# Optimization experiments

Measured on AMD Instinct MI355X. Metric: run time of the kernel, lower is better.

## Reference

```python
import jax, jax.numpy as jnp
import numpy as np

USER_NUM = 100000
ITEM_NUM = 50000
EMBED = 128
NUM_LAYERS = 3
N_INTERACTIONS = 1000000
BATCH = 16384


def setup_inputs() -> dict:
    key = jax.random.key(0)
    k1, k2 = jax.random.split(key)
    uEmbd = jax.random.normal(k1, (USER_NUM, EMBED), dtype=jnp.float32) * 0.01
    iEmbd = jax.random.normal(k2, (ITEM_NUM, EMBED), dtype=jnp.float32) * 0.01

    # Build symmetric normalized Laplacian L = D^-1/2 A D^-1/2 in COO form,
    # mirroring buildLaplacianMat (A holds ratings; D from binary degree).
    rng = np.random.default_rng(0)
    users = rng.integers(0, USER_NUM, N_INTERACTIONS)
    items = rng.integers(0, ITEM_NUM, N_INTERACTIONS)
    ratings = rng.integers(1, 6, N_INTERACTIONS).astype(np.float32)
    N = USER_NUM + ITEM_NUM
    row = np.concatenate([users, USER_NUM + items]).astype(np.int32)
    col = np.concatenate([USER_NUM + items, users]).astype(np.int32)
    vals = np.concatenate([ratings, ratings])
    deg = np.bincount(row, minlength=N).astype(np.float32)
    deg = np.maximum(deg, 1.0)
    vals = vals / np.sqrt(deg[row] * deg[col])

    k3, k4 = jax.random.split(jax.random.fold_in(key, 1))
    userIdx = jax.random.randint(k3, (BATCH,), 0, USER_NUM, dtype=jnp.int32)
    itemIdx = jax.random.randint(k4, (BATCH,), 0, ITEM_NUM, dtype=jnp.int32)

    return {
        "uEmbd": uEmbd,
        "iEmbd": iEmbd,
        "L_val": jnp.asarray(vals, dtype=jnp.float32),
        "L_row": jnp.asarray(row),
        "L_col": jnp.asarray(col),
        "userIdx": userIdx,
        "itemIdx": itemIdx,
    }


def reference(uEmbd, iEmbd, L_val, L_row, L_col, userIdx, itemIdx):
    userNum = uEmbd.shape[0]
    N = userNum + iEmbd.shape[0]
    # [N, d] stacked user+item embeddings
    feats = jnp.concatenate([uEmbd, iEmbd], axis=0)
    acc = feats  # running sum over layer outputs (layer 0 included)
    h = feats
    for _ in range(NUM_LAYERS):
        # SpMM: h <- L @ h via gather + segment-sum over COO edges
        h = jax.ops.segment_sum(L_val[:, None] * h[L_col], L_row, num_segments=N)
        acc = acc + h
    final = acc / jnp.asarray(NUM_LAYERS + 1, dtype=feats.dtype)
    u = final[userIdx]                       # [B, d]
    v = final[itemIdx + userNum]             # [B, d]
    return jnp.sum(u * v, axis=1)            # [B]
```

## Files before the change

### kernel.cpp

```cpp
#include <hip/hip_runtime.h>
#include <hip/hip_fp16.h>

#define EMBED 128
#define CHUNK 8
#define T_TILE 4096
#define NB_SH 10
#define BCAP 32768



__global__ __launch_bounds__(256) void passA(const int* __restrict__ row,
                                             const int* __restrict__ col,
                                             const float* __restrict__ val,
                                             int* __restrict__ bcnt,
                                             long long* __restrict__ bedges, int E) {
    __shared__ int sh_scan[256];
    __shared__ int sh_start[256];
    __shared__ int sh_cur[256];
    __shared__ int sh_base[256];
    __shared__ long long sh_data[T_TILE];
    __shared__ int sh_gpos[T_TILE];
    const int t0  = blockIdx.x * T_TILE;
    const int tid = threadIdx.x;

    sh_scan[tid] = 0;
    __syncthreads();
    #pragma unroll
    for (int i = 0; i < T_TILE / 256; ++i) {
        int idx = t0 + i * 256 + tid;
        if (idx < E) atomicAdd(&sh_scan[row[idx] >> NB_SH], 1);
    }
    __syncthreads();
    int x = sh_scan[tid];
    __syncthreads();
    for (int off = 1; off < 256; off <<= 1) {
        int t = (tid >= off) ? sh_scan[tid - off] : 0;
        __syncthreads();
        sh_scan[tid] += t;
        __syncthreads();
    }
    int excl = sh_scan[tid] - x;
    sh_start[tid] = excl;
    sh_cur[tid]   = excl;
    sh_base[tid]  = (x > 0) ? (tid * BCAP + atomicAdd(&bcnt[tid], x)) : 0;
    __syncthreads();
    #pragma unroll
    for (int i = 0; i < T_TILE / 256; ++i) {
        int idx = t0 + i * 256 + tid;
        if (idx < E) {
            int   r = row[idx];
            int   c = col[idx];
            float v = val[idx];
            int   b = r >> NB_SH;
            int   p = atomicAdd(&sh_cur[b], 1);
            unsigned lo = (unsigned)(((r & ((1 << NB_SH) - 1)) << 18) | c);
            sh_data[p] = ((long long)__float_as_int(v) << 32) | (long long)lo;
            sh_gpos[p] = sh_base[b] + (p - sh_start[b]);
        }
    }
    __syncthreads();
    int tot = sh_scan[255];
    for (int p = tid; p < tot; p += 256) {
        bedges[sh_gpos[p]] = sh_data[p];
    }
}


__global__ __launch_bounds__(1024) void passB(const long long* __restrict__ bedges,
                                              const int* __restrict__ bcnt,
                                              int* __restrict__ rs,
                                              int2* __restrict__ edges,
                                              int N, int E, int nbuckets) {
    __shared__ int sh_hist[1024];
    __shared__ int sh_scan[1024];
    __shared__ int sh_bc[256];
    __shared__ int sh_gbase;
    const int b    = blockIdx.x;
    const int tid  = threadIdx.x;
    const int base = b << NB_SH;
    const int cnt  = bcnt[b];
    const long long* seg = bedges + (size_t)b * BCAP;

    sh_hist[tid] = 0;
    if (tid < nbuckets) sh_bc[tid] = bcnt[tid];
    __syncthreads();
    if (tid == 0) {
        int g = 0;
        for (int j = 0; j < b; ++j) g += sh_bc[j];
        sh_gbase = g;
    }
    for (int k = tid; k < cnt; k += 1024) {
        unsigned lo = (unsigned)seg[k];
        atomicAdd(&sh_hist[lo >> 18], 1);
    }
    __syncthreads();
    int x = sh_hist[tid];
    sh_scan[tid] = x;
    __syncthreads();
    for (int off = 1; off < 1024; off <<= 1) {
        int t = (tid >= off) ? sh_scan[tid - off] : 0;
        __syncthreads();
        sh_scan[tid] += t;
        __syncthreads();
    }
    int excl = sh_scan[tid] - x;
    int gbase = sh_gbase;
    int rrow = base + tid;
    if (rrow < N) rs[rrow] = gbase + excl;
    if (b == nbuckets - 1 && tid == 0) rs[N] = E;
    sh_hist[tid] = excl;
    __syncthreads();
    for (int k = tid; k < cnt; k += 1024) {
        long long be = seg[k];
        unsigned lo = (unsigned)be;
        int p = atomicAdd(&sh_hist[lo >> 18], 1);
        edges[gbase + p] = make_int2((int)(lo & 0x3FFFF), (int)(be >> 32));
    }
}


__global__ void f32_to_i8_all(const float* __restrict__ uE, const float* __restrict__ iE,
                              unsigned* __restrict__ dst, float* __restrict__ sc,
                              int userNum, int N) {
    int gid  = blockIdx.x * blockDim.x + threadIdx.x;
    int wave = gid >> 6;
    int lane = threadIdx.x & 63;
    int half = lane >> 5;
    int l32  = lane & 31;
    int row  = wave * 2 + half;
    if (row >= N) return;
    const float* src = (row < userNum) ? (uE + (size_t)row * EMBED)
                                       : (iE + (size_t)(row - userNum) * EMBED);
    float4 a = *(const float4*)(src + 4 * l32);
    float am = fmaxf(fmaxf(fabsf(a.x), fabsf(a.y)), fmaxf(fabsf(a.z), fabsf(a.w)));
    #pragma unroll
    for (int off = 16; off > 0; off >>= 1)
        am = fmaxf(am, __shfl_xor(am, off));
    float s   = am * (1.f / 127.f);
    float inv = (am > 0.f) ? (127.f / am) : 0.f;
    int q0 = (int)rintf(a.x * inv) + 128;
    int q1 = (int)rintf(a.y * inv) + 128;
    int q2 = (int)rintf(a.z * inv) + 128;
    int q3 = (int)rintf(a.w * inv) + 128;
    unsigned w = (unsigned)q0 | ((unsigned)q1 << 8) | ((unsigned)q2 << 16)
               | ((unsigned)q3 << 24);
    dst[(size_t)row * 32 + l32] = w;
    if (l32 == 0) sc[row] = s;
}


#define GATHER_LOOP_I8(HSRC, SCSRC)                                           \
    for (int t = s; t < e; t += 32) {                                         \
        int ecl = t + l32;                                                    \
        ecl = (ecl < e) ? ecl : (e - 1);                                      \
        int2 myed = edges[ecl];                                               \
        float mvs = __int_as_float(myed.y) * SCSRC[myed.x];                   \
        int nb = e - t;                                                       \
        nb = (nb < 32) ? nb : 32;                                             \
        for (int k = 0; k < nb; k += CHUNK) {                                 \
            unsigned raw[CHUNK];                                              \
            float tv[CHUNK];                                                  \
            _Pragma("unroll")                                                 \
            for (int j = 0; j < CHUNK; ++j) {                                 \
                int   c  = __shfl(myed.x, k + j, 32);                         \
                float tj = __shfl(mvs, k + j, 32);                            \
                bool ok  = (k + j) < nb;                                      \
                tv[j]    = ok ? tj : 0.f;                                     \
                raw[j]   = HSRC[(size_t)c * 32 + l32];                        \
            }                                                                 \
            _Pragma("unroll")                                                 \
            for (int j = 0; j < CHUNK; ++j) {                                 \
                unsigned r = raw[j];                                          \
                float tj = tv[j];                                             \
                cb += tj;                                                     \
                acc.x = fmaf((float)(unsigned char)(r),       tj, acc.x);     \
                acc.y = fmaf((float)(unsigned char)(r >> 8),  tj, acc.y);     \
                acc.z = fmaf((float)(unsigned char)(r >> 16), tj, acc.z);     \
                acc.w = fmaf((float)(unsigned char)(r >> 24), tj, acc.w);     \
            }                                                                 \
        }                                                                     \
    }


__global__ void spmm_kernel(const int* __restrict__ rs, const int2* __restrict__ edges,
                            const unsigned* __restrict__ hin,
                            const float* __restrict__ scin,
                            unsigned* __restrict__ hout, float* __restrict__ scout,
                            int N) {
    int gid  = blockIdx.x * blockDim.x + threadIdx.x;
    int wave = gid >> 6;
    int lane = threadIdx.x & 63;
    int half = lane >> 5;
    int l32  = lane & 31;
    int row  = wave * 2 + half;
    if (row >= N) return;
    int s = rs[row], e = rs[row + 1];
    float4 acc = make_float4(0.f, 0.f, 0.f, 0.f);
    float cb = 0.f;

    GATHER_LOOP_I8(hin, scin)

    float b = 128.f * cb;
    acc.x -= b; acc.y -= b; acc.z -= b; acc.w -= b;
    float am = fmaxf(fmaxf(fabsf(acc.x), fabsf(acc.y)), fmaxf(fabsf(acc.z), fabsf(acc.w)));
    #pragma unroll
    for (int off = 16; off > 0; off >>= 1)
        am = fmaxf(am, __shfl_xor(am, off));
    float sq  = am * (1.f / 127.f);
    float inv = (am > 0.f) ? (127.f / am) : 0.f;
    int q0 = (int)rintf(acc.x * inv) + 128;
    int q1 = (int)rintf(acc.y * inv) + 128;
    int q2 = (int)rintf(acc.z * inv) + 128;
    int q3 = (int)rintf(acc.w * inv) + 128;
    unsigned w = (unsigned)q0 | ((unsigned)q1 << 8) | ((unsigned)q2 << 16)
               | ((unsigned)q3 << 24);
    hout[(size_t)row * 32 + l32] = w;
    if (l32 == 0) scout[row] = sq;
}


__global__ void spmm_pair(const int* __restrict__ rs, const int2* __restrict__ edges,
                          const unsigned* __restrict__ h1, const float* __restrict__ sc1,
                          const unsigned* __restrict__ h2, const float* __restrict__ sc2,
                          const float* __restrict__ uE, const float* __restrict__ iE,
                          const int* __restrict__ uIdx, const int* __restrict__ vIdx,
                          float* __restrict__ out, int B, int userNum) {
    int gid  = blockIdx.x * blockDim.x + threadIdx.x;
    int wave = gid >> 6;
    int lane = threadIdx.x & 63;
    int half = lane >> 5;
    int l32  = lane & 31;
    if (wave >= B) return;
    int row;
    const float* emb;
    if (half == 0) {
        int u = uIdx[wave];
        row = u;
        emb = uE + (size_t)u * EMBED;
    } else {
        int it = vIdx[wave];
        row = userNum + it;
        emb = iE + (size_t)it * EMBED;
    }
    float4 acc = *(const float4*)(emb + 4 * l32);
    {
        unsigned r1 = h1[(size_t)row * 32 + l32];
        unsigned r2 = h2[(size_t)row * 32 + l32];
        float s1 = sc1[row];
        float s2 = sc2[row];
        acc.x += ((float)(unsigned char)(r1)       - 128.f) * s1
               + ((float)(unsigned char)(r2)       - 128.f) * s2;
        acc.y += ((float)(unsigned char)(r1 >> 8)  - 128.f) * s1
               + ((float)(unsigned char)(r2 >> 8)  - 128.f) * s2;
        acc.z += ((float)(unsigned char)(r1 >> 16) - 128.f) * s1
               + ((float)(unsigned char)(r2 >> 16) - 128.f) * s2;
        acc.w += ((float)(unsigned char)(r1 >> 24) - 128.f) * s1
               + ((float)(unsigned char)(r2 >> 24) - 128.f) * s2;
    }
    float cb = 0.f;
    int s = rs[row], e = rs[row + 1];

    GATHER_LOOP_I8(h2, sc2)

    float b = 128.f * cb;
    acc.x -= b; acc.y -= b; acc.z -= b; acc.w -= b;

    float ox = __shfl_xor(acc.x, 32);
    float oy = __shfl_xor(acc.y, 32);
    float oz = __shfl_xor(acc.z, 32);
    float ow = __shfl_xor(acc.w, 32);
    float sdot = acc.x * ox + acc.y * oy + acc.z * oz + acc.w * ow;
    #pragma unroll
    for (int off = 16; off > 0; off >>= 1) sdot += __shfl_down(sdot, off, 32);
    sdot += __shfl_down(sdot, 32);
    if (lane == 0) out[wave] = sdot * (1.f / 32.f);
}


extern "C" void kernel_launch(void* const* d_in, const int* in_sizes, int n_in,
                              void* d_out, int out_size, void* d_ws, size_t ws_size,
                              hipStream_t stream) {
    const float* uE      = (const float*)d_in[0];
    const float* iE      = (const float*)d_in[1];
    const float* L_val   = (const float*)d_in[2];
    const int*   L_row   = (const int*)d_in[3];
    const int*   L_col   = (const int*)d_in[4];
    const int*   userIdx = (const int*)d_in[5];
    const int*   itemIdx = (const int*)d_in[6];

    const int userNum = in_sizes[0] / EMBED;
    const int itemNum = in_sizes[1] / EMBED;
    const int N = userNum + itemNum;
    const int E = in_sizes[2];
    const int B = in_sizes[5];
    float* out = (float*)d_out;

    char* ws = (char*)d_ws;
    size_t off = 0;
    auto alloc = [&](size_t bytes) -> void* {
        void* p = ws + off;
        off += (bytes + 1023) & ~(size_t)1023;
        return p;
    };
    const int NBUCKETS = (N + (1 << NB_SH) - 1) >> NB_SH;
    unsigned* h0 = (unsigned*)alloc((size_t)N * EMBED);
    unsigned* h1 = (unsigned*)alloc((size_t)N * EMBED);
    unsigned* h2 = (unsigned*)alloc((size_t)N * EMBED);
    float* sc0   = (float*)alloc((size_t)N * 4);
    float* sc1   = (float*)alloc((size_t)N * 4);
    float* sc2   = (float*)alloc((size_t)N * 4);
    int2*   edges  = (int2*) alloc((size_t)E * 8 + 256);
    long long* bedges = (long long*)alloc((size_t)NBUCKETS * BCAP * 8);
    int*    rs     = (int*)  alloc((size_t)(N + 1) * 4);
    int*    bcnt   = (int*)  alloc(1024);
    (void)off; (void)ws_size; (void)n_in; (void)out_size;

    const int tb = 256;

    (void)hipMemsetAsync(bcnt, 0, 1024, stream);
    passA<<<(E + T_TILE - 1) / T_TILE, 256, 0, stream>>>(L_row, L_col, L_val,
                                                         bcnt, bedges, E);
    passB<<<NBUCKETS, 1024, 0, stream>>>(bedges, bcnt, rs, edges, N, E, NBUCKETS);

    const int cv_blocks = (N + 7) / 8;
    f32_to_i8_all<<<cv_blocks, 256, 0, stream>>>(uE, iE, h0, sc0, userNum, N);

    const int spmm_blocks = (N + 7) / 8;
    spmm_kernel<<<spmm_blocks, 256, 0, stream>>>(rs, edges, h0, sc0, h1, sc1, N);
    spmm_kernel<<<spmm_blocks, 256, 0, stream>>>(rs, edges, h1, sc1, h2, sc2, N);

    spmm_pair<<<(B + 3) / 4, 256, 0, stream>>>(rs, edges, h1, sc1, h2, sc2, uE, iE,
                                               userIdx, itemIdx, out, B, userNum);
}
```

Baseline: 303.4 us.

## Merge SpMM layers into persistent kernel with grid barriers and fuse conversion into passA

The int8 conversion of the embeddings now runs as extra blocks inside the edge-bucketing kernel, which removes one launch. The two SpMM layers and the final pair-dot step are merged into one persistent kernel of 1024 blocks that loops over row-blocks and uses a software grid barrier (atomic counter plus spin) between phases. This replaces three launches and their gaps with in-kernel barriers. In exchange it relies on all 1024 blocks being co-resident and has fewer waves in flight per phase than the full launches had. The barrier counter is zeroed by widening the existing memset, which assumes the counter sits right after bcnt in the workspace.

```diff
diff --git a/kernel.cpp b/kernel.cpp
--- a/kernel.cpp
+++ b/kernel.cpp
@@ -6,22 +6,58 @@
 #define T_TILE 4096
 #define NB_SH 10
 #define BCAP 32768
-
-
-
-__global__ __launch_bounds__(256) void passA(const int* __restrict__ row,
-                                             const int* __restrict__ col,
-                                             const float* __restrict__ val,
-                                             int* __restrict__ bcnt,
-                                             long long* __restrict__ bedges, int E) {
+#define GRIDBLKS 1024
+
+
+
+__global__ __launch_bounds__(256) void passA_cvt(const int* __restrict__ row,
+                                                 const int* __restrict__ col,
+                                                 const float* __restrict__ val,
+                                                 int* __restrict__ bcnt,
+                                                 long long* __restrict__ bedges, int E,
+                                                 const float* __restrict__ uE,
+                                                 const float* __restrict__ iE,
+                                                 unsigned* __restrict__ h0,
+                                                 float* __restrict__ sc0,
+                                                 int userNum, int N, int CA) {
     __shared__ int sh_scan[256];
     __shared__ int sh_start[256];
     __shared__ int sh_cur[256];
     __shared__ int sh_base[256];
     __shared__ long long sh_data[T_TILE];
     __shared__ int sh_gpos[T_TILE];
-    const int t0  = blockIdx.x * T_TILE;
     const int tid = threadIdx.x;
+
+    if ((int)blockIdx.x >= CA) {
+        int vb   = (int)blockIdx.x - CA;
+        int gid  = vb * 256 + tid;
+        int wave = gid >> 6;
+        int lane = tid & 63;
+        int half = lane >> 5;
+        int l32  = lane & 31;
+        int r    = wave * 2 + half;
+        if (r >= N) return;
+        const float* src = (r < userNum) ? (uE + (size_t)r * EMBED)
+                                         : (iE + (size_t)(r - userNum) * EMBED);
+        float4 a = *(const float4*)(src + 4 * l32);
+        float am = fmaxf(fmaxf(fabsf(a.x), fabsf(a.y)), fmaxf(fabsf(a.z), fabsf(a.w)));
+        #pragma unroll
+        for (int off = 16; off > 0; off >>= 1)
+            am = fmaxf(am, __shfl_xor(am, off));
+        float s   = am * (1.f / 127.f);
+        float inv = (am > 0.f) ? (127.f / am) : 0.f;
+        int q0 = (int)rintf(a.x * inv) + 128;
+        int q1 = (int)rintf(a.y * inv) + 128;
+        int q2 = (int)rintf(a.z * inv) + 128;
+        int q3 = (int)rintf(a.w * inv) + 128;
+        unsigned w = (unsigned)q0 | ((unsigned)q1 << 8) | ((unsigned)q2 << 16)
+                   | ((unsigned)q3 << 24);
+        h0[(size_t)r * 32 + l32] = w;
+        if (l32 == 0) sc0[r] = s;
+        return;
+    }
+
+    const int t0 = blockIdx.x * T_TILE;
 
     sh_scan[tid] = 0;
     __syncthreads();
@@ -116,36 +152,6 @@
         int p = atomicAdd(&sh_hist[lo >> 18], 1);
         edges[gbase + p] = make_int2((int)(lo & 0x3FFFF), (int)(be >> 32));
     }
-}
-
-
-__global__ void f32_to_i8_all(const float* __restrict__ uE, const float* __restrict__ iE,
-                              unsigned* __restrict__ dst, float* __restrict__ sc,
-                              int userNum, int N) {
-    int gid  = blockIdx.x * blockDim.x + threadIdx.x;
-    int wave = gid >> 6;
-    int lane = threadIdx.x & 63;
-    int half = lane >> 5;
-    int l32  = lane & 31;
-    int row  = wave * 2 + half;
-    if (row >= N) return;
-    const float* src = (row < userNum) ? (uE + (size_t)row * EMBED)
-                                       : (iE + (size_t)(row - userNum) * EMBED);
-    float4 a = *(const float4*)(src + 4 * l32);
-    float am = fmaxf(fmaxf(fabsf(a.x), fabsf(a.y)), fmaxf(fabsf(a.z), fabsf(a.w)));
-    #pragma unroll
-    for (int off = 16; off > 0; off >>= 1)
-        am = fmaxf(am, __shfl_xor(am, off));
-    float s   = am * (1.f / 127.f);
-    float inv = (am > 0.f) ? (127.f / am) : 0.f;
-    int q0 = (int)rintf(a.x * inv) + 128;
-    int q1 = (int)rintf(a.y * inv) + 128;
-    int q2 = (int)rintf(a.z * inv) + 128;
-    int q3 = (int)rintf(a.w * inv) + 128;
-    unsigned w = (unsigned)q0 | ((unsigned)q1 << 8) | ((unsigned)q2 << 16)
-               | ((unsigned)q3 << 24);
-    dst[(size_t)row * 32 + l32] = w;
-    if (l32 == 0) sc[row] = s;
 }
 
 
@@ -182,14 +188,14 @@
     }
 
 
-__global__ void spmm_kernel(const int* __restrict__ rs, const int2* __restrict__ edges,
-                            const unsigned* __restrict__ hin,
-                            const float* __restrict__ scin,
-                            unsigned* __restrict__ hout, float* __restrict__ scout,
-                            int N) {
-    int gid  = blockIdx.x * blockDim.x + threadIdx.x;
+__device__ __forceinline__ void spmm_rows(int gid, const int* __restrict__ rs,
+                                          const int2* __restrict__ edges,
+                                          const unsigned* __restrict__ hin,
+                                          const float* __restrict__ scin,
+                                          unsigned* __restrict__ hout,
+                                          float* __restrict__ scout, int N) {
     int wave = gid >> 6;
-    int lane = threadIdx.x & 63;
+    int lane = gid & 63;
     int half = lane >> 5;
     int l32  = lane & 31;
     int row  = wave * 2 + half;
@@ -218,16 +224,19 @@
     if (l32 == 0) scout[row] = sq;
 }
 
-
-__global__ void spmm_pair(const int* __restrict__ rs, const int2* __restrict__ edges,
-                          const unsigned* __restrict__ h1, const float* __restrict__ sc1,
-                          const unsigned* __restrict__ h2, const float* __restrict__ sc2,
-                          const float* __restrict__ uE, const float* __restrict__ iE,
-                          const int* __restrict__ uIdx, const int* __restrict__ vIdx,
-                          float* __restrict__ out, int B, int userNum) {
-    int gid  = blockIdx.x * blockDim.x + threadIdx.x;
+__device__ __forceinline__ void pair_rows(int gid, const int* __restrict__ rs,
+                                          const int2* __restrict__ edges,
+                                          const unsigned* __restrict__ h1,
+                                          const float* __restrict__ sc1,
+                                          const unsigned* __restrict__ h2,
+                                          const float* __restrict__ sc2,
+                                          const float* __restrict__ uE,
+                                          const float* __restrict__ iE,
+                                          const int* __restrict__ uIdx,
+                                          const int* __restrict__ vIdx,
+                                          float* __restrict__ out, int B, int userNum) {
     int wave = gid >> 6;
-    int lane = threadIdx.x & 63;
+    int lane = gid & 63;
     int half = lane >> 5;
     int l32  = lane & 31;
     if (wave >= B) return;
@@ -274,6 +283,44 @@
     for (int off = 16; off > 0; off >>= 1) sdot += __shfl_down(sdot, off, 32);
     sdot += __shfl_down(sdot, 32);
     if (lane == 0) out[wave] = sdot * (1.f / 32.f);
+}
+
+
+__device__ __forceinline__ void gridbar(int* bar, int target) {
+    __syncthreads();
+    if (threadIdx.x == 0) {
+        __threadfence();
+        atomicAdd(bar, 1);
+        while (__hip_atomic_load(bar, __ATOMIC_ACQUIRE,
+                                 __HIP_MEMORY_SCOPE_AGENT) < target)
+            __builtin_amdgcn_s_sleep(2);
+        __threadfence();
+    }
+    __syncthreads();
+}
+
+
+__global__ __launch_bounds__(256, 4) void spmm_mega(
+        const int* __restrict__ rs, const int2* __restrict__ edges,
+        const unsigned* __restrict__ h0, const float* __restrict__ sc0,
+        unsigned* __restrict__ h1, float* __restrict__ sc1,
+        unsigned* __restrict__ h2, float* __restrict__ sc2,
+        const float* __restrict__ uE, const float* __restrict__ iE,
+        const int* __restrict__ uIdx, const int* __restrict__ vIdx,
+        float* __restrict__ out, int B, int userNum, int N,
+        int* __restrict__ bar) {
+    const int tid = threadIdx.x;
+    const int nvb = (N + 7) / 8;
+    for (int vb = blockIdx.x; vb < nvb; vb += gridDim.x)
+        spmm_rows(vb * 256 + tid, rs, edges, h0, sc0, h1, sc1, N);
+    gridbar(bar, gridDim.x);
+    for (int vb = blockIdx.x; vb < nvb; vb += gridDim.x)
+        spmm_rows(vb * 256 + tid, rs, edges, h1, sc1, h2, sc2, N);
+    gridbar(bar, 2 * gridDim.x);
+    const int npb = (B + 3) / 4;
+    for (int vb = blockIdx.x; vb < npb; vb += gridDim.x)
+        pair_rows(vb * 256 + tid, rs, edges, h1, sc1, h2, sc2, uE, iE,
+                  uIdx, vIdx, out, B, userNum);
 }
 
 
@@ -313,22 +360,18 @@
     long long* bedges = (long long*)alloc((size_t)NBUCKETS * BCAP * 8);
     int*    rs     = (int*)  alloc((size_t)(N + 1) * 4);
     int*    bcnt   = (int*)  alloc(1024);
+    int*    bar    = (int*)  alloc(1024);
     (void)off; (void)ws_size; (void)n_in; (void)out_size;
 
-    const int tb = 256;
-
-    (void)hipMemsetAsync(bcnt, 0, 1024, stream);
-    passA<<<(E + T_TILE - 1) / T_TILE, 256, 0, stream>>>(L_row, L_col, L_val,
-                                                         bcnt, bedges, E);
+    (void)hipMemsetAsync(bcnt, 0, 2048, stream);
+
+    const int CA  = (E + T_TILE - 1) / T_TILE;
+    const int CVB = (N + 7) / 8;
+    passA_cvt<<<CA + CVB, 256, 0, stream>>>(L_row, L_col, L_val, bcnt, bedges, E,
+                                            uE, iE, h0, sc0, userNum, N, CA);
     passB<<<NBUCKETS, 1024, 0, stream>>>(bedges, bcnt, rs, edges, N, E, NBUCKETS);
 
-    const int cv_blocks = (N + 7) / 8;
-    f32_to_i8_all<<<cv_blocks, 256, 0, stream>>>(uE, iE, h0, sc0, userNum, N);
-
-    const int spmm_blocks = (N + 7) / 8;
-    spmm_kernel<<<spmm_blocks, 256, 0, stream>>>(rs, edges, h0, sc0, h1, sc1, N);
-    spmm_kernel<<<spmm_blocks, 256, 0, stream>>>(rs, edges, h1, sc1, h2, sc2, N);
-
-    spmm_pair<<<(B + 3) / 4, 256, 0, stream>>>(rs, edges, h1, sc1, h2, sc2, uE, iE,
-                                               userIdx, itemIdx, out, B, userNum);
-}
+    spmm_mega<<<GRIDBLKS, 256, 0, stream>>>(rs, edges, h0, sc0, h1, sc1, h2, sc2,
+                                            uE, iE, userIdx, itemIdx, out,
+                                            B, userNum, N, bar);
+}
```

Result: slower. 848.8 us (+179.7%).

## Replace bucketed two-pass CSR build with degree count, scan, and atomic scatter

Applied to the files above, without the earlier changes.

Swaps the shared-memory bucketed two-pass COO-to-CSR conversion for a global atomic degree histogram, a single-block prefix scan, and an atomic-cursor scatter of edges. The int8 embedding conversion is fused into the degree-count kernel as extra blocks, which removes one launch. The new build avoids the intermediate bucket buffer but relies on many global atomics. It also runs a serial single-block scan over 150k rows and leaves edge order within each row nondeterministic, so float summation order can vary between runs.

```diff
diff --git a/kernel.cpp b/kernel.cpp
--- a/kernel.cpp
+++ b/kernel.cpp
@@ -3,149 +3,117 @@
 
 #define EMBED 128
 #define CHUNK 8
-#define T_TILE 4096
-#define NB_SH 10
-#define BCAP 32768
-
-
-
-__global__ __launch_bounds__(256) void passA(const int* __restrict__ row,
-                                             const int* __restrict__ col,
-                                             const float* __restrict__ val,
-                                             int* __restrict__ bcnt,
-                                             long long* __restrict__ bedges, int E) {
-    __shared__ int sh_scan[256];
-    __shared__ int sh_start[256];
-    __shared__ int sh_cur[256];
-    __shared__ int sh_base[256];
-    __shared__ long long sh_data[T_TILE];
-    __shared__ int sh_gpos[T_TILE];
-    const int t0  = blockIdx.x * T_TILE;
+
+
+
+__global__ __launch_bounds__(256) void count_cvt(const int* __restrict__ row,
+                                                 int* __restrict__ deg, int E, int CC,
+                                                 const float* __restrict__ uE,
+                                                 const float* __restrict__ iE,
+                                                 unsigned* __restrict__ h0,
+                                                 float* __restrict__ sc0,
+                                                 int userNum, int N) {
     const int tid = threadIdx.x;
-
-    sh_scan[tid] = 0;
-    __syncthreads();
-    #pragma unroll
-    for (int i = 0; i < T_TILE / 256; ++i) {
-        int idx = t0 + i * 256 + tid;
-        if (idx < E) atomicAdd(&sh_scan[row[idx] >> NB_SH], 1);
-    }
-    __syncthreads();
-    int x = sh_scan[tid];
-    __syncthreads();
-    for (int off = 1; off < 256; off <<= 1) {
-        int t = (tid >= off) ? sh_scan[tid - off] : 0;
-        __syncthreads();
-        sh_scan[tid] += t;
-        __syncthreads();
-    }
-    int excl = sh_scan[tid] - x;
-    sh_start[tid] = excl;
-    sh_cur[tid]   = excl;
-    sh_base[tid]  = (x > 0) ? (tid * BCAP + atomicAdd(&bcnt[tid], x)) : 0;
-    __syncthreads();
-    #pragma unroll
-    for (int i = 0; i < T_TILE / 256; ++i) {
-        int idx = t0 + i * 256 + tid;
-        if (idx < E) {
-            int   r = row[idx];
-            int   c = col[idx];
-            float v = val[idx];
-            int   b = r >> NB_SH;
-            int   p = atomicAdd(&sh_cur[b], 1);
-            unsigned lo = (unsigned)(((r & ((1 << NB_SH) - 1)) << 18) | c);
-            sh_data[p] = ((long long)__float_as_int(v) << 32) | (long long)lo;
-            sh_gpos[p] = sh_base[b] + (p - sh_start[b]);
+    if ((int)blockIdx.x >= CC) {
+        int vb   = (int)blockIdx.x - CC;
+        int gid  = vb * 256 + tid;
+        int wave = gid >> 6;
+        int lane = tid & 63;
+        int half = lane >> 5;
+        int l32  = lane & 31;
+        int r    = wave * 2 + half;
+        if (r >= N) return;
+        const float* src = (r < userNum) ? (uE + (size_t)r * EMBED)
+                                         : (iE + (size_t)(r - userNum) * EMBED);
+        float4 a = *(const float4*)(src + 4 * l32);
+        float am = fmaxf(fmaxf(fabsf(a.x), fabsf(a.y)), fmaxf(fabsf(a.z), fabsf(a.w)));
+        #pragma unroll
+        for (int off = 16; off > 0; off >>= 1)
+            am = fmaxf(am, __shfl_xor(am, off));
+        float s   = am * (1.f / 127.f);
+        float inv = (am > 0.f) ? (127.f / am) : 0.f;
+        int q0 = (int)rintf(a.x * inv) + 128;
+        int q1 = (int)rintf(a.y * inv) + 128;
+        int q2 = (int)rintf(a.z * inv) + 128;
+        int q3 = (int)rintf(a.w * inv) + 128;
+        unsigned w = (unsigned)q0 | ((unsigned)q1 << 8) | ((unsigned)q2 << 16)
+                   | ((unsigned)q3 << 24);
+        h0[(size_t)r * 32 + l32] = w;
+        if (l32 == 0) sc0[r] = s;
+        return;
+    }
+    int base = ((int)blockIdx.x * 256 + tid) * 4;
+    if (base + 3 < E) {
+        int4 r4 = *(const int4*)(row + base);
+        atomicAdd(&deg[r4.x], 1);
+        atomicAdd(&deg[r4.y], 1);
+        atomicAdd(&deg[r4.z], 1);
+        atomicAdd(&deg[r4.w], 1);
+    } else {
+        for (int j = 0; j < 4; ++j) {
+            int idx = base + j;
+            if (idx < E) atomicAdd(&deg[row[idx]], 1);
         }
     }
-    __syncthreads();
-    int tot = sh_scan[255];
-    for (int p = tid; p < tot; p += 256) {
-        bedges[sh_gpos[p]] = sh_data[p];
-    }
-}
-
-
-__global__ __launch_bounds__(1024) void passB(const long long* __restrict__ bedges,
-                                              const int* __restrict__ bcnt,
-                                              int* __restrict__ rs,
-                                              int2* __restrict__ edges,
-                                              int N, int E, int nbuckets) {
-    __shared__ int sh_hist[1024];
-    __shared__ int sh_scan[1024];
-    __shared__ int sh_bc[256];
-    __shared__ int sh_gbase;
-    const int b    = blockIdx.x;
-    const int tid  = threadIdx.x;
-    const int base = b << NB_SH;
-    const int cnt  = bcnt[b];
-    const long long* seg = bedges + (size_t)b * BCAP;
-
-    sh_hist[tid] = 0;
-    if (tid < nbuckets) sh_bc[tid] = bcnt[tid];
-    __syncthreads();
-    if (tid == 0) {
-        int g = 0;
-        for (int j = 0; j < b; ++j) g += sh_bc[j];
-        sh_gbase = g;
-    }
-    for (int k = tid; k < cnt; k += 1024) {
-        unsigned lo = (unsigned)seg[k];
-        atomicAdd(&sh_hist[lo >> 18], 1);
-    }
-    __syncthreads();
-    int x = sh_hist[tid];
-    sh_scan[tid] = x;
+}
+
+
+__global__ __launch_bounds__(1024) void scan_deg(const int* __restrict__ deg,
+                                                 int* __restrict__ rs,
+                                                 int* __restrict__ cursor,
+                                                 int N, int E) {
+    __shared__ int part[1024];
+    const int tid = threadIdx.x;
+    const int per = (N + 1023) / 1024;
+    int lo = tid * per;
+    int hi = lo + per; if (hi > N) hi = N;
+    int sum = 0;
+    for (int i = lo; i < hi; ++i) sum += deg[i];
+    part[tid] = sum;
     __syncthreads();
     for (int off = 1; off < 1024; off <<= 1) {
-        int t = (tid >= off) ? sh_scan[tid - off] : 0;
+        int t = (tid >= off) ? part[tid - off] : 0;
         __syncthreads();
-        sh_scan[tid] += t;
+        part[tid] += t;
         __syncthreads();
     }
-    int excl = sh_scan[tid] - x;
-    int gbase = sh_gbase;
-    int rrow = base + tid;
-    if (rrow < N) rs[rrow] = gbase + excl;
-    if (b == nbuckets - 1 && tid == 0) rs[N] = E;
-    sh_hist[tid] = excl;
-    __syncthreads();
-    for (int k = tid; k < cnt; k += 1024) {
-        long long be = seg[k];
-        unsigned lo = (unsigned)be;
-        int p = atomicAdd(&sh_hist[lo >> 18], 1);
-        edges[gbase + p] = make_int2((int)(lo & 0x3FFFF), (int)(be >> 32));
-    }
-}
-
-
-__global__ void f32_to_i8_all(const float* __restrict__ uE, const float* __restrict__ iE,
-                              unsigned* __restrict__ dst, float* __restrict__ sc,
-                              int userNum, int N) {
-    int gid  = blockIdx.x * blockDim.x + threadIdx.x;
-    int wave = gid >> 6;
-    int lane = threadIdx.x & 63;
-    int half = lane >> 5;
-    int l32  = lane & 31;
-    int row  = wave * 2 + half;
-    if (row >= N) return;
-    const float* src = (row < userNum) ? (uE + (size_t)row * EMBED)
-                                       : (iE + (size_t)(row - userNum) * EMBED);
-    float4 a = *(const float4*)(src + 4 * l32);
-    float am = fmaxf(fmaxf(fabsf(a.x), fabsf(a.y)), fmaxf(fabsf(a.z), fabsf(a.w)));
-    #pragma unroll
-    for (int off = 16; off > 0; off >>= 1)
-        am = fmaxf(am, __shfl_xor(am, off));
-    float s   = am * (1.f / 127.f);
-    float inv = (am > 0.f) ? (127.f / am) : 0.f;
-    int q0 = (int)rintf(a.x * inv) + 128;
-    int q1 = (int)rintf(a.y * inv) + 128;
-    int q2 = (int)rintf(a.z * inv) + 128;
-    int q3 = (int)rintf(a.w * inv) + 128;
-    unsigned w = (unsigned)q0 | ((unsigned)q1 << 8) | ((unsigned)q2 << 16)
-               | ((unsigned)q3 << 24);
-    dst[(size_t)row * 32 + l32] = w;
-    if (l32 == 0) sc[row] = s;
+    int run = part[tid] - sum;
+    for (int i = lo; i < hi; ++i) {
+        rs[i] = run;
+        cursor[i] = run;
+        run += deg[i];
+    }
+    if (tid == 1023) rs[N] = E;
+}
+
+
+__global__ __launch_bounds__(256) void scatter_edges(const int* __restrict__ row,
+                                                     const int* __restrict__ col,
+                                                     const float* __restrict__ val,
+                                                     int* __restrict__ cursor,
+                                                     int2* __restrict__ edges, int E) {
+    int base = ((int)blockIdx.x * 256 + threadIdx.x) * 4;
+    if (base + 3 < E) {
+        int4   r4 = *(const int4*)(row + base);
+        int4   c4 = *(const int4*)(col + base);
+        float4 v4 = *(const float4*)(val + base);
+        int p0 = atomicAdd(&cursor[r4.x], 1);
+        int p1 = atomicAdd(&cursor[r4.y], 1);
+        int p2 = atomicAdd(&cursor[r4.z], 1);
+        int p3 = atomicAdd(&cursor[r4.w], 1);
+        edges[p0] = make_int2(c4.x, __float_as_int(v4.x));
+        edges[p1] = make_int2(c4.y, __float_as_int(v4.y));
+        edges[p2] = make_int2(c4.z, __float_as_int(v4.z));
+        edges[p3] = make_int2(c4.w, __float_as_int(v4.w));
+    } else {
+        for (int j = 0; j < 4; ++j) {
+            int idx = base + j;
+            if (idx < E) {
+                int p = atomicAdd(&cursor[row[idx]], 1);
+                edges[p] = make_int2(col[idx], __float_as_int(val[idx]));
+            }
+        }
+    }
 }
 
 
@@ -302,28 +270,26 @@
         off += (bytes + 1023) & ~(size_t)1023;
         return p;
     };
-    const int NBUCKETS = (N + (1 << NB_SH) - 1) >> NB_SH;
     unsigned* h0 = (unsigned*)alloc((size_t)N * EMBED);
     unsigned* h1 = (unsigned*)alloc((size_t)N * EMBED);
     unsigned* h2 = (unsigned*)alloc((size_t)N * EMBED);
     float* sc0   = (float*)alloc((size_t)N * 4);
     float* sc1   = (float*)alloc((size_t)N * 4);
     float* sc2   = (float*)alloc((size_t)N * 4);
-    int2*   edges  = (int2*) alloc((size_t)E * 8 + 256);
-    long long* bedges = (long long*)alloc((size_t)NBUCKETS * BCAP * 8);
-    int*    rs     = (int*)  alloc((size_t)(N + 1) * 4);
-    int*    bcnt   = (int*)  alloc(1024);
+    int2*  edges = (int2*) alloc((size_t)E * 8 + 256);
+    int*   rs    = (int*)  alloc((size_t)(N + 1) * 4);
+    int*   deg   = (int*)  alloc((size_t)(N + 1) * 4);
+    int*   cursor= (int*)  alloc((size_t)(N + 1) * 4);
     (void)off; (void)ws_size; (void)n_in; (void)out_size;
 
-    const int tb = 256;
-
-    (void)hipMemsetAsync(bcnt, 0, 1024, stream);
-    passA<<<(E + T_TILE - 1) / T_TILE, 256, 0, stream>>>(L_row, L_col, L_val,
-                                                         bcnt, bedges, E);
-    passB<<<NBUCKETS, 1024, 0, stream>>>(bedges, bcnt, rs, edges, N, E, NBUCKETS);
-
-    const int cv_blocks = (N + 7) / 8;
-    f32_to_i8_all<<<cv_blocks, 256, 0, stream>>>(uE, iE, h0, sc0, userNum, N);
+    (void)hipMemsetAsync(deg, 0, (size_t)N * 4, stream);
+
+    const int CC  = (E + 1023) / 1024;
+    const int CVB = (N + 7) / 8;
+    count_cvt<<<CC + CVB, 256, 0, stream>>>(L_row, deg, E, CC,
+                                            uE, iE, h0, sc0, userNum, N);
+    scan_deg<<<1, 1024, 0, stream>>>(deg, rs, cursor, N, E);
+    scatter_edges<<<CC, 256, 0, stream>>>(L_row, L_col, L_val, cursor, edges, E);
 
     const int spmm_blocks = (N + 7) / 8;
     spmm_kernel<<<spmm_blocks, 256, 0, stream>>>(rs, edges, h0, sc0, h1, sc1, N);
```

After: 808.4 us. +166.4%, slower.
